# Performance work log

Hardware: AMD Instinct MI355X
Metric: run time of the kernel (lower is better)

Reference implementation:

```python
import jax, jax.numpy as jnp
import numpy as np

B, SEQ, DIM = 2, 2048, 1024
HEADS, HEAD_DIM = 16, 64
HIDDEN = 2816
EPS = 1e-5
LN_EPS = 1e-5


def rmsnorm(x, w, eps=EPS):
    return x * jax.lax.rsqrt(jnp.mean(x * x, axis=-1, keepdims=True) + eps) * w


def layernorm(x, w, b, eps=LN_EPS):
    mu = jnp.mean(x, axis=-1, keepdims=True)
    var = jnp.mean((x - mu) ** 2, axis=-1, keepdims=True)
    return (x - mu) * jax.lax.rsqrt(var + eps) * w + b


def modulate(x, shift, scale):
    # x: [B,S,D], shift/scale: [B,D]
    return x * (1.0 + scale[:, None, :]) + shift[:, None, :]


def apply_rope(t, cos, sin):
    # t: [B,S,H,D]; cos/sin: [S, D/2] -> complex multiply on (even,odd) pairs
    t = t.reshape(*t.shape[:-1], HEAD_DIM // 2, 2)
    t0, t1 = t[..., 0], t[..., 1]
    c = cos[None, :, None, :]
    s = sin[None, :, None, :]
    o0 = t0 * c - t1 * s
    o1 = t0 * s + t1 * c
    return jnp.stack([o0, o1], axis=-1).reshape(*t.shape[:-2], HEAD_DIM)


def setup_inputs() -> dict:
    key = jax.random.key(0)
    ks = jax.random.split(key, 12)
    def w(k, shape, s=0.02):
        return jax.random.normal(k, shape, dtype=jnp.float32) * s
    x = jax.random.normal(ks[0], (B, SEQ, DIM), dtype=jnp.float32)
    adaln_input = jax.random.normal(ks[1], (B, DIM), dtype=jnp.float32)
    pos = jnp.arange(SEQ, dtype=jnp.float32)
    inv_freq = 1.0 / (10000.0 ** (jnp.arange(0, HEAD_DIM, 2, dtype=jnp.float32) / HEAD_DIM))
    ang = pos[:, None] * inv_freq[None, :]  # [S, D/2]
    return dict(
        x=x, adaln_input=adaln_input,
        freqs_cos=jnp.cos(ang), freqs_sin=jnp.sin(ang),
        wq=w(ks[2], (DIM, DIM)), wk=w(ks[3], (DIM, DIM)),
        wv=w(ks[4], (DIM, DIM)), wo=w(ks[5], (DIM, DIM)),
        q_norm_w=jnp.ones(DIM, jnp.float32), q_norm_b=jnp.zeros(DIM, jnp.float32),
        k_norm_w=jnp.ones(DIM, jnp.float32), k_norm_b=jnp.zeros(DIM, jnp.float32),
        attn_norm_w=jnp.ones(DIM, jnp.float32), ffn_norm_w=jnp.ones(DIM, jnp.float32),
        ada_w=w(ks[6], (DIM, 6 * DIM)), ada_b=jnp.zeros(6 * DIM, jnp.float32),
        w1=w(ks[7], (DIM, HIDDEN)), w2=w(ks[8], (HIDDEN, DIM)), w3=w(ks[9], (DIM, HIDDEN)),
    )


def reference(x, adaln_input, freqs_cos, freqs_sin, wq, wk, wv, wo,
              q_norm_w, q_norm_b, k_norm_w, k_norm_b,
              attn_norm_w, ffn_norm_w, ada_w, ada_b, w1, w2, w3):
    # adaLN modulation: SiLU -> Linear -> 6 chunks of [B, DIM]
    m = jax.nn.silu(adaln_input) @ ada_w + ada_b
    shift_msa, scale_msa, gate_msa, shift_mlp, scale_mlp, gate_mlp = jnp.split(m, 6, axis=1)

    # --- attention branch ---
    h = modulate(rmsnorm(x, attn_norm_w), shift_msa, scale_msa)
    xq = layernorm(h @ wq, q_norm_w, q_norm_b)
    xk = layernorm(h @ wk, k_norm_w, k_norm_b)
    xv = h @ wv
    xq = xq.reshape(B, SEQ, HEADS, HEAD_DIM)
    xk = xk.reshape(B, SEQ, HEADS, HEAD_DIM)
    xv = xv.reshape(B, SEQ, HEADS, HEAD_DIM)
    xq = apply_rope(xq, freqs_cos, freqs_sin)
    xk = apply_rope(xk, freqs_cos, freqs_sin)
    scale = 1.0 / jnp.sqrt(jnp.float32(HEAD_DIM))
    scores = jnp.einsum('bshd,bthd->bhst', xq, xk) * scale  # [B,H,S,S]
    probs = jax.nn.softmax(scores, axis=-1)
    attn = jnp.einsum('bhst,bthd->bshd', probs, xv).reshape(B, SEQ, DIM)
    attn = attn @ wo
    x = x + gate_msa[:, None, :] * attn

    # --- MLP branch (SwiGLU) ---
    h = modulate(rmsnorm(x, ffn_norm_w), shift_mlp, scale_mlp)
    ffn = (jax.nn.silu(h @ w1) * (h @ w3)) @ w2
    x = x + gate_mlp[:, None, :] * ffn
    return x
```

## Files before the change

kernel.cpp:

```cpp
#include <hip/hip_runtime.h>
#include <hip/hip_bf16.h>

#define B_   2
#define S_   2048
#define D_   1024
#define H_   16
#define HD_  64
#define HID_ 2816

typedef unsigned short u16;
typedef unsigned int   u32;
typedef __attribute__((ext_vector_type(8))) short short8;
typedef __attribute__((ext_vector_type(4))) float f32x4;
typedef __attribute__((ext_vector_type(4))) u32   u32x4;
typedef __attribute__((ext_vector_type(2))) unsigned uvec2;

static __device__ __forceinline__ float bf2f(u16 u){ return __uint_as_float(((u32)u)<<16); }
static __device__ __forceinline__ u16 f2bf(float f){
  u32 u = __float_as_uint(f);
  u32 r = (u + 0x7FFFu + ((u>>16)&1u)) >> 16;
  return (u16)r;
}
static __device__ __forceinline__ u16 f2bfr(float f){
  return (u16)((__float_as_uint(f) + 0x8000u) >> 16);
}
static __device__ __forceinline__ u32 pk2(float a, float b){
  return ((__float_as_uint(a) + 0x8000u) >> 16) | ((__float_as_uint(b) + 0x8000u) & 0xFFFF0000u);
}
static __device__ __forceinline__ u32 cvtpk(float lo, float hi){
  u32 r; asm("v_cvt_pk_bf16_f32 %0, %1, %2" : "=v"(r) : "v"(lo), "v"(hi)); return r;
}
static __device__ __forceinline__ float vmax3(float a, float b, float c){
  float d; asm("v_max3_f32 %0, %1, %2, %3" : "=v"(d) : "v"(a), "v"(b), "v"(c)); return d;
}
static __device__ __forceinline__ void plswap16(float x, float& a, float& b){
#if __has_builtin(__builtin_amdgcn_permlane16_swap)
  uvec2 r = __builtin_amdgcn_permlane16_swap(__float_as_uint(x), __float_as_uint(x), false, false);
  a = __uint_as_float(r[0]); b = __uint_as_float(r[1]);
#else
  a = x; b = __shfl_xor(x, 16, 64);
#endif
}
static __device__ __forceinline__ void plswap32(float x, float& a, float& b){
#if __has_builtin(__builtin_amdgcn_permlane32_swap)
  uvec2 r = __builtin_amdgcn_permlane32_swap(__float_as_uint(x), __float_as_uint(x), false, false);
  a = __uint_as_float(r[0]); b = __uint_as_float(r[1]);
#else
  a = x; b = __shfl_xor(x, 32, 64);
#endif
}

static __device__ __forceinline__ void ld4(const u16* p, float* v){
  ushort4 t = *reinterpret_cast<const ushort4*>(p);
  v[0]=bf2f(t.x); v[1]=bf2f(t.y); v[2]=bf2f(t.z); v[3]=bf2f(t.w);
}
static __device__ __forceinline__ void ld4(const float* p, float* v){
  float4 t = *reinterpret_cast<const float4*>(p);
  v[0]=t.x; v[1]=t.y; v[2]=t.z; v[3]=t.w;
}
static __device__ __forceinline__ void st4(u16* p, const float* v){
  ushort4 t; t.x=f2bf(v[0]); t.y=f2bf(v[1]); t.z=f2bf(v[2]); t.w=f2bf(v[3]);
  *reinterpret_cast<ushort4*>(p)=t;
}

static __device__ __forceinline__ float ld1g(const void* p, size_t i, bool f32){
  return f32 ? ((const float*)p)[i] : bf2f(((const u16*)p)[i]);
}
static __device__ __forceinline__ void ld4g(const void* p, size_t i, float* v, bool f32){
  if(f32){
    float4 t = *reinterpret_cast<const float4*>((const float*)p + i);
    v[0]=t.x; v[1]=t.y; v[2]=t.z; v[3]=t.w;
  }else{
    ushort4 t = *reinterpret_cast<const ushort4*>((const u16*)p + i);
    v[0]=bf2f(t.x); v[1]=bf2f(t.y); v[2]=bf2f(t.z); v[3]=bf2f(t.w);
  }
}
static __device__ __forceinline__ void st4g(void* p, size_t i, const float* v, bool f32){
  if(f32){
    float4 t; t.x=v[0]; t.y=v[1]; t.z=v[2]; t.w=v[3];
    *reinterpret_cast<float4*>((float*)p + i) = t;
  }else{
    st4((u16*)p + i, v);
  }
}

static __device__ __forceinline__ void gl2lds16(const u16* g, const u16* l){
  typedef __attribute__((address_space(3))) u16 lds_u16;
  typedef const __attribute__((address_space(1))) u16 glb_u16;
  __builtin_amdgcn_global_load_lds((glb_u16*)(uintptr_t)g,
                                   (lds_u16*)(u32)(uintptr_t)l, 16, 0, 0);
}

__global__ __launch_bounds__(256) void k_probe_zero(const u16* fc_raw, int* flag, float* m){
  int i = blockIdx.x*256 + threadIdx.x;
  if(i < 12288) m[i] = 0.f;
  if(i == 0) *flag = (fc_raw[0]==0) ? 1 : 0;
}

static __device__ __forceinline__ float blk_sum(float v, float* red){
  #pragma unroll
  for(int o=32;o;o>>=1) v += __shfl_xor(v,o,64);
  int lane = threadIdx.x & 63, w = threadIdx.x >> 6;
  if(lane==0) red[w]=v;
  __syncthreads();
  float t = red[0]+red[1]+red[2]+red[3];
  __syncthreads();
  return t;
}

__global__ __launch_bounds__(256) void k_adaln(const void* a, const void* W, const void* bias,
                                               float* m, const int* flag){
  bool f32 = flag[0] != 0;
  __shared__ float sl[2][128];
  int bk = blockIdx.y;
  {
    int bb = threadIdx.x >> 7, kk = threadIdx.x & 127;
    float x = ld1g(a, bb*D_ + bk*128 + kk, f32);
    sl[bb][kk] = x/(1.f+__expf(-x));
  }
  __syncthreads();
  int n = blockIdx.x*256 + threadIdx.x;
  float p0 = 0.f, p1 = 0.f;
  for(int kk=0;kk<128;kk++){
    float w = ld1g(W, (size_t)(bk*128+kk)*6144 + n, f32);
    p0 += sl[0][kk]*w; p1 += sl[1][kk]*w;
  }
  if(bk==0){ float bv = ld1g(bias, n, f32); p0 += bv; p1 += bv; }
  atomicAdd(&m[n], p0);
  atomicAdd(&m[6144+n], p1);
}

__global__ __launch_bounds__(256) void k_rms_mod(const void* x, const void* nw, const float* m,
                                                 u16* h, int shift_off, int scale_off,
                                                 const int* flag){
  bool f32 = flag[0] != 0;
  __shared__ float red[4];
  int row = blockIdx.x; int b = row >> 11;
  int d0 = threadIdx.x*4;
  float v[4]; ld4g(x, (size_t)row*D_ + d0, v, f32);
  float ss = v[0]*v[0]+v[1]*v[1]+v[2]*v[2]+v[3]*v[3];
  float tot = blk_sum(ss, red);
  float r = rsqrtf(tot*(1.f/D_) + 1e-5f);
  const float* mb = m + b*6144;
  float wn[4]; ld4g(nw, d0, wn, f32);
  float o[4];
  #pragma unroll
  for(int j=0;j<4;j++){
    int d = d0+j;
    o[j] = v[j]*r*wn[j]*(1.f+mb[scale_off+d]) + mb[shift_off+d];
  }
  st4(h + (size_t)row*D_ + d0, o);
}

__global__ __launch_bounds__(256) void k_resid_rms(const void* x, const u16* y, const float* m,
                                                   const void* nw, float* x2, u16* h,
                                                   const int* flag){
  bool f32 = flag[0] != 0;
  __shared__ float red[4];
  int row = blockIdx.x; int b = row >> 11;
  int d0 = threadIdx.x*4;
  size_t i4 = (size_t)row*D_ + d0;
  float xv[4], yv[4];
  ld4g(x, i4, xv, f32); ld4(y+i4, yv);
  const float* mb = m + b*6144;
  float v[4];
  #pragma unroll
  for(int j=0;j<4;j++) v[j] = xv[j] + mb[2048+d0+j]*yv[j];
  float4 t; t.x=v[0]; t.y=v[1]; t.z=v[2]; t.w=v[3];
  *reinterpret_cast<float4*>(x2+i4) = t;
  float ss = v[0]*v[0]+v[1]*v[1]+v[2]*v[2]+v[3]*v[3];
  float tot = blk_sum(ss, red);
  float r = rsqrtf(tot*(1.f/D_) + 1e-5f);
  float wn[4]; ld4g(nw, d0, wn, f32);
  float o[4];
  #pragma unroll
  for(int j=0;j<4;j++)
    o[j] = v[j]*r*wn[j]*(1.f+mb[4096+d0+j]) + mb[3072+d0+j];
  st4(h + i4, o);
}

__global__ __launch_bounds__(256) void k_ln_rope2(u16* t, const void* qw, const void* qb,
                                                  const void* kw, const void* kb2,
                                                  const void* fc, const void* fs, const int* flag){
  bool f32 = flag[0] != 0;
  __shared__ float red[4];
  int row = blockIdx.x; int s = row & (S_-1);
  const void* w  = blockIdx.y ? kw  : qw;
  const void* bb = blockIdx.y ? kb2 : qb;
  int d0 = threadIdx.x*4;
  u16* tp = t + (size_t)row*3072 + blockIdx.y*1024 + d0;
  float v[4]; ld4(tp, v);
  float sm = v[0]+v[1]+v[2]+v[3];
  float sq = v[0]*v[0]+v[1]*v[1]+v[2]*v[2]+v[3]*v[3];
  float tsm = blk_sum(sm, red);
  float tsq = blk_sum(sq, red);
  float mu  = tsm*(1.f/D_);
  float var = tsq*(1.f/D_) - mu*mu;
  float rs  = rsqrtf(var + 1e-5f);
  float wv[4], bv[4]; ld4g(w, d0, wv, f32); ld4g(bb, d0, bv, f32);
  float y[4];
  #pragma unroll
  for(int j=0;j<4;j++) y[j] = (v[j]-mu)*rs*wv[j] + bv[j];
  int pos = d0 & 63; int i0 = pos>>1;
  float c0 = ld1g(fc, s*32+i0,   f32), s0 = ld1g(fs, s*32+i0,   f32);
  float c1 = ld1g(fc, s*32+i0+1, f32), s1 = ld1g(fs, s*32+i0+1, f32);
  float o[4];
  o[0] = y[0]*c0 - y[1]*s0;
  o[1] = y[0]*s0 + y[1]*c0;
  o[2] = y[2]*c1 - y[3]*s1;
  o[3] = y[2]*s1 + y[3]*c1;
  st4(tp, o);
}

__global__ __launch_bounds__(256) void k_wt3(const void* W0, const void* W1, const void* W2,
                                             u16* WT, int Kd, int Nd, const int* flag){
  bool f32 = flag[0] != 0;
  const void* W = blockIdx.z==0 ? W0 : (blockIdx.z==1 ? W1 : W2);
  u16* dst_base = WT + (size_t)blockIdx.z * (size_t)Kd * Nd;
  __shared__ u16 L[64][72];
  int tid = threadIdx.x;
  int k0 = blockIdx.x*64, n0 = blockIdx.y*64;
  int r = tid>>2, c0 = (tid&3)*16;
  if(f32){
    const float* Wf = (const float*)W;
    #pragma unroll
    for(int j=0;j<4;j++){
      float4 t = *reinterpret_cast<const float4*>(&Wf[(size_t)(k0+r)*Nd + n0 + c0 + j*4]);
      L[r][c0+j*4+0]=f2bfr(t.x); L[r][c0+j*4+1]=f2bfr(t.y);
      L[r][c0+j*4+2]=f2bfr(t.z); L[r][c0+j*4+3]=f2bfr(t.w);
    }
  }else{
    const u16* Wh = (const u16*)W;
    *reinterpret_cast<short8*>(&L[r][c0]) =
      *reinterpret_cast<const short8*>(&Wh[(size_t)(k0+r)*Nd + n0 + c0]);
    *reinterpret_cast<short8*>(&L[r][c0+8]) =
      *reinterpret_cast<const short8*>(&Wh[(size_t)(k0+r)*Nd + n0 + c0 + 8]);
  }
  __syncthreads();
  int n = tid>>2, kk0 = (tid&3)*16;
  u16 tmp[16];
  #pragma unroll
  for(int j=0;j<16;j++) tmp[j] = L[kk0+j][n];
  u16* dst = dst_base + (size_t)(n0+n)*Kd + k0 + kk0;
  *reinterpret_cast<short8*>(dst)   = *reinterpret_cast<const short8*>(tmp);
  *reinterpret_cast<short8*>(dst+8) = *reinterpret_cast<const short8*>(tmp+8);
}

__global__ __launch_bounds__(256) void k_wt13(const void* W1, const void* W3,
                                              u16* WT, const int* flag){
  bool f32 = flag[0] != 0;
  const int Kd = 1024, Nd = HID_;
  const void* W = blockIdx.z ? W3 : W1;
  int radd = blockIdx.z ? 32 : 0;
  __shared__ u16 L[64][72];
  int tid = threadIdx.x;
  int k0 = blockIdx.x*64, n0 = blockIdx.y*64;
  int r = tid>>2, c0 = (tid&3)*16;
  if(f32){
    const float* Wf = (const float*)W;
    #pragma unroll
    for(int j=0;j<4;j++){
      float4 t = *reinterpret_cast<const float4*>(&Wf[(size_t)(k0+r)*Nd + n0 + c0 + j*4]);
      L[r][c0+j*4+0]=f2bfr(t.x); L[r][c0+j*4+1]=f2bfr(t.y);
      L[r][c0+j*4+2]=f2bfr(t.z); L[r][c0+j*4+3]=f2bfr(t.w);
    }
  }else{
    const u16* Wh = (const u16*)W;
    *reinterpret_cast<short8*>(&L[r][c0]) =
      *reinterpret_cast<const short8*>(&Wh[(size_t)(k0+r)*Nd + n0 + c0]);
    *reinterpret_cast<short8*>(&L[r][c0+8]) =
      *reinterpret_cast<const short8*>(&Wh[(size_t)(k0+r)*Nd + n0 + c0 + 8]);
  }
  __syncthreads();
  int n = tid>>2, kk0 = (tid&3)*16;
  u16 tmp[16];
  #pragma unroll
  for(int j=0;j<16;j++) tmp[j] = L[kk0+j][n];
  int nglob = n0 + n;
  int rw = ((nglob>>5)<<6) + (nglob&31) + radd;
  u16* dst = WT + (size_t)rw*Kd + k0 + kk0;
  *reinterpret_cast<short8*>(dst)   = *reinterpret_cast<const short8*>(tmp);
  *reinterpret_cast<short8*>(dst+8) = *reinterpret_cast<const short8*>(tmp+8);
}

template<int TM, int EPI>
__global__ __launch_bounds__(256) void k_gemm_mfma(const u16* A, int lda, const u16* BT, int ldb,
                                                   u16* C, int N, int K,
                                                   const float* x2, const float* mg,
                                                   void* outp, const int* flag){
  __shared__ __align__(16) u16 As[TM*64];
  __shared__ __align__(16) u16 Bs[128*64];
  int tid = threadIdx.x, lane = tid&63, w = tid>>6;
  int col = lane&15, quad = lane>>4;
  int row0 = blockIdx.y*TM, col0 = blockIdx.x*128;
  const u16* Ab = A  + (size_t)row0*lda;
  const u16* Bb = BT + (size_t)col0*ldb;
  constexpr int MI = TM/32;
  int wm = (w>>1)*(TM/2);
  int wn = (w&1)*64;
  f32x4 acc[MI][4];
  #pragma unroll
  for(int i=0;i<MI;i++)
    #pragma unroll
    for(int j=0;j<4;j++) acc[i][j] = (f32x4){0.f,0.f,0.f,0.f};

  for(int k0=0;k0<K;k0+=64){
    __syncthreads();
    #pragma unroll
    for(int i=0;i<TM/32;i++){
      int c = i*256 + w*64 + lane;
      int r = c>>3, s = c&7, gs = s ^ (r&7);
      gl2lds16(Ab + (size_t)r*lda + k0 + gs*8, As + (size_t)c*8);
    }
    #pragma unroll
    for(int i=0;i<4;i++){
      int c = i*256 + w*64 + lane;
      int r = c>>3, s = c&7, gs = s ^ (r&7);
      gl2lds16(Bb + (size_t)r*ldb + k0 + gs*8, Bs + (size_t)c*8);
    }
    __syncthreads();
    #pragma unroll
    for(int ks=0;ks<64;ks+=32){
      short8 af[MI], bfr[4];
      #pragma unroll
      for(int mi=0;mi<MI;mi++){
        int r = wm+mi*16+col;
        int sch = ((ks>>3) + quad) ^ (col&7);
        af[mi] = *reinterpret_cast<const short8*>(&As[r*64 + sch*8]);
      }
      #pragma unroll
      for(int ni=0;ni<4;ni++){
        int r = wn+ni*16+col;
        int sch = ((ks>>3) + quad) ^ (col&7);
        bfr[ni] = *reinterpret_cast<const short8*>(&Bs[r*64 + sch*8]);
      }
      #pragma unroll
      for(int mi=0;mi<MI;mi++)
        #pragma unroll
        for(int ni=0;ni<4;ni++)
          acc[mi][ni] = __builtin_amdgcn_mfma_f32_16x16x32_bf16(af[mi], bfr[ni], acc[mi][ni], 0,0,0);
    }
  }
  if constexpr(EPI==0){
    #pragma unroll
    for(int mi=0;mi<MI;mi++)
      #pragma unroll
      for(int r=0;r<4;r++){
        size_t rowoff = (size_t)(row0+wm+mi*16+quad*4+r)*N + col0 + wn;
        #pragma unroll
        for(int ni=0;ni<4;ni++)
          C[rowoff + ni*16 + col] = f2bfr(acc[mi][ni][r]);
      }
  } else if constexpr(EPI==1){
    int cb = blockIdx.x*64 + (wn?32:0) + col;
    #pragma unroll
    for(int mi=0;mi<MI;mi++)
      #pragma unroll
      for(int r=0;r<4;r++){
        int row = row0+wm+mi*16+quad*4+r;
        u16* gp = C + (size_t)row*HID_ + cb;
        #pragma unroll
        for(int ni=0;ni<2;ni++){
          float a = acc[mi][ni][r], cc = acc[mi][ni+2][r];
          float sv = a * __builtin_amdgcn_rcpf(1.f + __builtin_amdgcn_exp2f(-1.4426950f*a));
          gp[ni*16] = f2bfr(sv*cc);
        }
      }
  } else {
    bool f32o = flag[0] != 0;
    #pragma unroll
    for(int mi=0;mi<MI;mi++)
      #pragma unroll
      for(int r=0;r<4;r++){
        int row = row0+wm+mi*16+quad*4+r;
        int b = row >> 11;
        #pragma unroll
        for(int ni=0;ni<4;ni++){
          int cc = col0 + wn + ni*16 + col;
          float v = x2[(size_t)row*D_ + cc] + mg[b*6144 + 5120 + cc]*acc[mi][ni][r];
          if(f32o) ((float*)outp)[(size_t)row*D_ + cc] = v;
          else     ((u16*)outp)[(size_t)row*D_ + cc]   = f2bfr(v);
        }
      }
  }
}

__global__ __launch_bounds__(256) void k_vt(const u16* v, int vstr, u16* vt){
  __shared__ u16 L[64][72];
  int tid = threadIdx.x;
  int wg = blockIdx.x;
  int kblk = wg & 31; int bh = wg >> 5; int h = bh & 15, b = bh >> 4;
  int row = tid>>2, c0 = (tid&3)*16;
  const u16* src = v + (size_t)(b*S_ + kblk*64 + row)*vstr + h*HD_ + c0;
  *reinterpret_cast<short8*>(&L[row][c0])   = *reinterpret_cast<const short8*>(src);
  *reinterpret_cast<short8*>(&L[row][c0+8]) = *reinterpret_cast<const short8*>(src+8);
  __syncthreads();
  int hd = tid>>2, k0 = (tid&3)*16;
  u16 tmp[16];
  #pragma unroll
  for(int j=0;j<16;j++) tmp[j] = L[k0+j][hd];
  u16* dst = vt + ((size_t)bh*HD_ + hd)*S_ + kblk*64 + k0;
  *reinterpret_cast<short8*>(dst)   = *reinterpret_cast<const short8*>(tmp);
  *reinterpret_cast<short8*>(dst+8) = *reinterpret_cast<const short8*>(tmp+8);
}

__global__ __launch_bounds__(256) void k_attn_mfma(const u16* q, const u16* k, const u16* vt,
                                                   u16* o, int qks){
  __shared__ __align__(16) u16 Ks[2][64*64];
  __shared__ __align__(16) u16 Vs[2][64*64];
  int tid = threadIdx.x, lane = tid & 63, wid = tid >> 6;
  int col = lane & 15, quad = lane >> 4;
  int c7 = col & 7;
  int wg = blockIdx.x;
  int qblk = wg & 31; int bh = wg >> 5; int h = bh & 15, b = bh >> 4;

  const u16* kb  = k  + (size_t)b*S_*qks + h*HD_;
  const u16* vtb = vt + (size_t)bh*HD_*S_;

  short8 qa0, qa1;
  {
    const float qscale = 0.18033688f;
    const u16* qp = q + (size_t)(b*S_ + qblk*64 + wid*16 + col)*qks + h*HD_ + quad*8;
    short8 t0 = *reinterpret_cast<const short8*>(qp);
    short8 t1 = *reinterpret_cast<const short8*>(qp + 32);
    #pragma unroll
    for(int j=0;j<8;j++){
      qa0[j] = (short)f2bf(bf2f((u16)t0[j])*qscale);
      qa1[j] = (short)f2bf(bf2f((u16)t1[j])*qscale);
    }
  }
  float m_i = -1e30f, l_i = 0.f;
  f32x4 acc[4];
  #pragma unroll
  for(int t=0;t<4;t++) acc[t] = (f32x4){0.f,0.f,0.f,0.f};

  int l0 = tid>>3;
  int l1 = 32 + l0;
  int gs = ((tid&7) ^ (l0&7))*8;
  int kl0 = 32*(l0>>5) + 8*((l0>>2)&3) + 4*((l0>>4)&1) + (l0&3);
  int kl1 = 32*(l1>>5) + 8*((l1>>2)&3) + 4*((l1>>4)&1) + (l1&3);
  const u16* kp0 = kb + (size_t)kl0*qks + gs;
  const u16* kp1 = kb + (size_t)kl1*qks + gs;
  const u16* vp0 = vtb + (size_t)l0*S_ + gs;
  const u16* vp1 = vtb + (size_t)l1*S_ + gs;

  gl2lds16(kp0, &Ks[0][tid*8]);
  gl2lds16(kp1, &Ks[0][2048 + tid*8]);
  gl2lds16(vp0, &Vs[0][tid*8]);
  gl2lds16(vp1, &Vs[0][2048 + tid*8]);

  for(int i=0;i<32;i++){
    __syncthreads();
    const u16* Kc = Ks[i&1];
    const u16* Vc = Vs[i&1];
    if(i < 31){
      size_t off = (size_t)(i+1)*64;
      u16* Kn = (u16*)Ks[(i+1)&1];
      u16* Vn = (u16*)Vs[(i+1)&1];
      gl2lds16(kp0 + off*qks, &Kn[tid*8]);
      gl2lds16(kp1 + off*qks, &Kn[2048 + tid*8]);
      gl2lds16(vp0 + off,     &Vn[tid*8]);
      gl2lds16(vp1 + off,     &Vn[2048 + tid*8]);
    }

    f32x4 st[4];
    #pragma unroll
    for(int mt=0;mt<4;mt++){
      st[mt] = (f32x4){0.f,0.f,0.f,0.f};
      short8 ka0 = *reinterpret_cast<const short8*>(&Kc[(mt*16+col)*64 + ((quad  ) ^ c7)*8]);
      short8 ka1 = *reinterpret_cast<const short8*>(&Kc[(mt*16+col)*64 + ((quad+4) ^ c7)*8]);
      st[mt] = __builtin_amdgcn_mfma_f32_16x16x32_bf16(ka0, qa0, st[mt], 0,0,0);
      st[mt] = __builtin_amdgcn_mfma_f32_16x16x32_bf16(ka1, qa1, st[mt], 0,0,0);
    }
    float t0 = vmax3(st[0][0], st[0][1], st[0][2]);
    float t1 = vmax3(st[0][3], st[1][0], st[1][1]);
    float t2 = vmax3(st[1][2], st[1][3], st[2][0]);
    float t3 = vmax3(st[2][1], st[2][2], st[2][3]);
    float t4 = vmax3(st[3][0], st[3][1], st[3][2]);
    float cm = fmaxf(vmax3(t0, t1, t2), vmax3(t3, t4, st[3][3]));
    { float a, bb2; plswap16(cm, a, bb2); cm = fmaxf(a, bb2);
      plswap32(cm, a, bb2); cm = fmaxf(a, bb2); }
    if(__any(cm > m_i)){
      float mn = fmaxf(m_i, cm);
      float al = __builtin_amdgcn_exp2f(m_i - mn);
      m_i = mn;
      l_i *= al;
      #pragma unroll
      for(int t=0;t<4;t++) acc[t] *= al;
    }
    float pe[4][4];
    #pragma unroll
    for(int mt=0;mt<4;mt++)
      #pragma unroll
      for(int r=0;r<4;r++) pe[mt][r] = __builtin_amdgcn_exp2f(st[mt][r]-m_i);
    #pragma unroll
    for(int w=0;w<2;w++){
      u32x4 pw;
      pw[0] = cvtpk(pe[2*w][0],   pe[2*w][1]);
      pw[1] = cvtpk(pe[2*w][2],   pe[2*w][3]);
      pw[2] = cvtpk(pe[2*w+1][0], pe[2*w+1][1]);
      pw[3] = cvtpk(pe[2*w+1][2], pe[2*w+1][3]);
      short8 pb = *reinterpret_cast<short8*>(&pw);
      #pragma unroll
      for(int ht=0;ht<4;ht++){
        short8 vf = *reinterpret_cast<const short8*>(&Vc[(ht*16+col)*64 + ((w*4+quad) ^ c7)*8]);
        acc[ht] = __builtin_amdgcn_mfma_f32_16x16x32_bf16(vf, pb, acc[ht], 0,0,0);
      }
    }
    float s0 = (pe[0][0]+pe[0][1]) + (pe[0][2]+pe[0][3]);
    float s1 = (pe[1][0]+pe[1][1]) + (pe[1][2]+pe[1][3]);
    float s2 = (pe[2][0]+pe[2][1]) + (pe[2][2]+pe[2][3]);
    float s3 = (pe[3][0]+pe[3][1]) + (pe[3][2]+pe[3][3]);
    l_i += (s0+s1) + (s2+s3);
  }
  { float a, bb2; plswap16(l_i, a, bb2); l_i = a + bb2;
    plswap32(l_i, a, bb2); l_i = a + bb2; }
  float inv = __builtin_amdgcn_rcpf(l_i);
  u16* ob = o + (size_t)(b*S_ + qblk*64 + wid*16 + col)*D_ + h*HD_;
  #pragma unroll
  for(int ht=0;ht<4;ht++){
    uint2 t;
    t.x = cvtpk(acc[ht][0]*inv, acc[ht][1]*inv);
    t.y = cvtpk(acc[ht][2]*inv, acc[ht][3]*inv);
    *reinterpret_cast<uint2*>(ob + ht*16 + quad*4) = t;
  }
}

extern "C" void kernel_launch(void* const* d_in, const int* in_sizes, int n_in,
                              void* d_out, int out_size, void* d_ws, size_t ws_size,
                              hipStream_t stream){
  const void* x   = d_in[0];
  const void* ada = d_in[1];
  const void* fc  = d_in[2];
  const void* fs  = d_in[3];
  const void* wq  = d_in[4];
  const void* wk  = d_in[5];
  const void* wv  = d_in[6];
  const void* wo  = d_in[7];
  const void* qnw = d_in[8];
  const void* qnb = d_in[9];
  const void* knw = d_in[10];
  const void* knb = d_in[11];
  const void* anw = d_in[12];
  const void* fnw = d_in[13];
  const void* aw  = d_in[14];
  const void* ab  = d_in[15];
  const void* w1  = d_in[16];
  const void* w2  = d_in[17];
  const void* w3  = d_in[18];
  char* ws = (char*)d_ws;
  const size_t MB = 1u<<20;

  int*   flag = (int*)ws;
  float* m    = (float*)(ws + 4096);
  u16*  hbuf  = (u16*)(ws + 1*MB);
  u16*  xqkv  = (u16*)(ws + 9*MB);
  float* x2   = (float*)(ws + 9*MB);
  u16*  proj  = (u16*)(ws + 25*MB);
  u16*  wreg  = (u16*)(ws + 33*MB);
  u16*  g     = (u16*)(ws + 45*MB);
  u16*  vt    = wreg;

  dim3 blk(256);

  k_probe_zero<<<dim3(48), blk, 0, stream>>>((const u16*)fc, flag, m);
  k_adaln<<<dim3(24,8), blk, 0, stream>>>(ada, aw, ab, m, flag);
  k_rms_mod<<<dim3(B_*S_), blk, 0, stream>>>(x, anw, m, hbuf, 0, 1024, flag);

  k_wt3<<<dim3(16,16,3), blk, 0, stream>>>(wq, wk, wv, wreg, 1024, 1024, flag);
  k_gemm_mfma<128,0><<<dim3(24,32), blk, 0, stream>>>(hbuf, 1024, wreg, 1024, xqkv,
                                                      3072, 1024, nullptr, nullptr, nullptr, flag);

  k_ln_rope2<<<dim3(B_*S_,2), blk, 0, stream>>>(xqkv, qnw, qnb, knw, knb, fc, fs, flag);
  k_vt<<<dim3(B_*H_*S_/64), blk, 0, stream>>>(xqkv + 2048, 3072, vt);
  k_attn_mfma<<<dim3(B_*H_*S_/64), blk, 0, stream>>>(xqkv, xqkv + 1024, vt, hbuf, 3072);

  k_wt3<<<dim3(16,16,1), blk, 0, stream>>>(wo, wo, wo, wreg, 1024, 1024, flag);
  k_gemm_mfma<64,0><<<dim3(8,64), blk, 0, stream>>>(hbuf, 1024, wreg, 1024, proj,
                                                    1024, 1024, nullptr, nullptr, nullptr, flag);
  k_resid_rms<<<dim3(B_*S_), blk, 0, stream>>>(x, proj, m, fnw, x2, hbuf, flag);

  k_wt13<<<dim3(16,44,2), blk, 0, stream>>>(w1, w3, wreg, flag);
  k_gemm_mfma<128,1><<<dim3(44,32), blk, 0, stream>>>(hbuf, 1024, wreg, 1024, g,
                                                      5632, 1024, nullptr, nullptr, nullptr, flag);
  k_wt3<<<dim3(44,16,1), blk, 0, stream>>>(w2, w2, w2, wreg, 2816, 1024, flag);
  k_gemm_mfma<64,2><<<dim3(8,64), blk, 0, stream>>>(g, 2816, wreg, 2816, nullptr,
                                                    1024, 2816, x2, m, d_out, flag);
}
```

Measured before the change: 442.0 us.

## Compute softmax row sums via MFMA, lazy rescale, packed subtract, block remap

```diff
diff --git a/kernel.cpp b/kernel.cpp
--- a/kernel.cpp
+++ b/kernel.cpp
@@ -12,6 +12,7 @@
 typedef unsigned int   u32;
 typedef __attribute__((ext_vector_type(8))) short short8;
 typedef __attribute__((ext_vector_type(4))) float f32x4;
+typedef __attribute__((ext_vector_type(2))) float f32x2;
 typedef __attribute__((ext_vector_type(4))) u32   u32x4;
 typedef __attribute__((ext_vector_type(2))) unsigned uvec2;
 
@@ -32,6 +33,9 @@
 }
 static __device__ __forceinline__ float vmax3(float a, float b, float c){
   float d; asm("v_max3_f32 %0, %1, %2, %3" : "=v"(d) : "v"(a), "v"(b), "v"(c)); return d;
+}
+static __device__ __forceinline__ f32x2 pkadd(f32x2 a, f32x2 b){
+  f32x2 d; asm("v_pk_add_f32 %0, %1, %2" : "=v"(d) : "v"(a), "v"(b)); return d;
 }
 static __device__ __forceinline__ void plswap16(float x, float& a, float& b){
 #if __has_builtin(__builtin_amdgcn_permlane16_swap)
@@ -411,7 +415,7 @@
   int tid = threadIdx.x, lane = tid & 63, wid = tid >> 6;
   int col = lane & 15, quad = lane >> 4;
   int c7 = col & 7;
-  int wg = blockIdx.x;
+  int wg = ((blockIdx.x & 7) << 7) + (blockIdx.x >> 3);
   int qblk = wg & 31; int bh = wg >> 5; int h = bh & 15, b = bh >> 4;
 
   const u16* kb  = k  + (size_t)b*S_*qks + h*HD_;
@@ -429,7 +433,13 @@
       qa1[j] = (short)f2bf(bf2f((u16)t1[j])*qscale);
     }
   }
-  float m_i = -1e30f, l_i = 0.f;
+  short8 vone;
+  #pragma unroll
+  for(int j=0;j<8;j++) vone[j] = (short)0x3F80;
+
+  float m_i = -1e30f;
+  f32x2 nm = (f32x2){1e30f, 1e30f};
+  f32x4 accl = (f32x4){0.f,0.f,0.f,0.f};
   f32x4 acc[4];
   #pragma unroll
   for(int t=0;t<4;t++) acc[t] = (f32x4){0.f,0.f,0.f,0.f};
@@ -480,19 +490,25 @@
     float cm = fmaxf(vmax3(t0, t1, t2), vmax3(t3, t4, st[3][3]));
     { float a, bb2; plswap16(cm, a, bb2); cm = fmaxf(a, bb2);
       plswap32(cm, a, bb2); cm = fmaxf(a, bb2); }
-    if(__any(cm > m_i)){
+    if(__any(cm - m_i > 8.f)){
       float mn = fmaxf(m_i, cm);
       float al = __builtin_amdgcn_exp2f(m_i - mn);
       m_i = mn;
-      l_i *= al;
+      nm = (f32x2){-mn, -mn};
+      accl[0] *= al;
       #pragma unroll
       for(int t=0;t<4;t++) acc[t] *= al;
     }
     float pe[4][4];
     #pragma unroll
-    for(int mt=0;mt<4;mt++)
-      #pragma unroll
-      for(int r=0;r<4;r++) pe[mt][r] = __builtin_amdgcn_exp2f(st[mt][r]-m_i);
+    for(int mt=0;mt<4;mt++){
+      f32x2 lo = pkadd(st[mt].xy, nm);
+      f32x2 hi = pkadd(st[mt].zw, nm);
+      pe[mt][0] = __builtin_amdgcn_exp2f(lo.x);
+      pe[mt][1] = __builtin_amdgcn_exp2f(lo.y);
+      pe[mt][2] = __builtin_amdgcn_exp2f(hi.x);
+      pe[mt][3] = __builtin_amdgcn_exp2f(hi.y);
+    }
     #pragma unroll
     for(int w=0;w<2;w++){
       u32x4 pw;
@@ -506,16 +522,10 @@
         short8 vf = *reinterpret_cast<const short8*>(&Vc[(ht*16+col)*64 + ((w*4+quad) ^ c7)*8]);
         acc[ht] = __builtin_amdgcn_mfma_f32_16x16x32_bf16(vf, pb, acc[ht], 0,0,0);
       }
-    }
-    float s0 = (pe[0][0]+pe[0][1]) + (pe[0][2]+pe[0][3]);
-    float s1 = (pe[1][0]+pe[1][1]) + (pe[1][2]+pe[1][3]);
-    float s2 = (pe[2][0]+pe[2][1]) + (pe[2][2]+pe[2][3]);
-    float s3 = (pe[3][0]+pe[3][1]) + (pe[3][2]+pe[3][3]);
-    l_i += (s0+s1) + (s2+s3);
-  }
-  { float a, bb2; plswap16(l_i, a, bb2); l_i = a + bb2;
-    plswap32(l_i, a, bb2); l_i = a + bb2; }
-  float inv = __builtin_amdgcn_rcpf(l_i);
+      accl = __builtin_amdgcn_mfma_f32_16x16x32_bf16(vone, pb, accl, 0,0,0);
+    }
+  }
+  float inv = __builtin_amdgcn_rcpf(accl[0]);
   u16* ob = o + (size_t)(b*S_ + qblk*64 + wid*16 + col)*D_ + h*HD_;
   #pragma unroll
   for(int ht=0;ht<4;ht++){
```

Result: no change. 439.0 us (-0.7%).
